# Kernel tuning notes

Measured on AMD Instinct MI355X. Metric: run time of the kernel, lower is better.

The kernel has to match this reference:

```python
import jax, jax.numpy as jnp
import numpy as np

EPS = 1e-6

def _feature_map(x):
    # elu(x) + 1, from https://arxiv.org/pdf/2006.16236.pdf
    return jax.nn.elu(x) + 1.0

def setup_inputs() -> dict:
    key = jax.random.key(0)
    kq, kk, kv = jax.random.split(key, 3)
    N, S, H, D = 4, 4096, 8, 64
    queries = jax.random.normal(kq, (N, S, H, D), dtype=jnp.float32)
    keys = jax.random.normal(kk, (N, S, H, D), dtype=jnp.float32)
    values = jax.random.normal(kv, (N, S, H, D), dtype=jnp.float32)
    q_mask = jnp.ones((N, S), dtype=bool)
    kv_mask = jnp.ones((N, S), dtype=bool)
    return {"queries": queries, "keys": keys, "values": values,
            "q_mask": q_mask, "kv_mask": kv_mask}

def reference(queries, keys, values, q_mask, kv_mask):
    dt = queries.dtype
    q = _feature_map(queries) * q_mask[:, :, None, None].astype(dt)
    k = _feature_map(keys) * kv_mask[:, :, None, None].astype(dt)
    v = values * kv_mask[:, :, None, None].astype(dt)
    L = v.shape[1]
    v = v / L  # normalize for numerical stability, rescaled at the end
    # kv: [N,H,D,V] outer-product aggregation over S2
    kv = jnp.einsum('nshd,nshv->nhdv', k, v)
    # z: [N,L,H] normalizer
    z = 1.0 / (jnp.einsum('nlhd,nhd->nlh', q, k.sum(axis=1)) + EPS)
    out = jnp.einsum('nlhd,nhdv->nlhv', q, kv) * z[..., None] * L
    return out
```

## Files before the change

### kernel.cpp

```cpp
#include <hip/hip_runtime.h>

#define NB    4
#define SEQ   4096
#define NH    8
#define DIM   64
#define NPAIR (NB * NH)
#define SC    256
#define NT    (SC / 64)
#define NCHUNK (SEQ / SC)
#define NLT   (SEQ / 64)
#define VSTR  (NH * DIM)

#define EPSF  1e-6f

__device__ __forceinline__ float fm(float x) {
    return x > 0.0f ? x + 1.0f : __expf(x);
}

#define FMA4(AI, KS) \
    acc[AI][0] = fmaf((KS), v4.x, acc[AI][0]); \
    acc[AI][1] = fmaf((KS), v4.y, acc[AI][1]); \
    acc[AI][2] = fmaf((KS), v4.z, acc[AI][2]); \
    acc[AI][3] = fmaf((KS), v4.w, acc[AI][3]);

template<int ATOMIC>
__global__ __launch_bounds__(256, 2) void la_phase1(
    const float* __restrict__ Kp, const float* __restrict__ Vp,
    float* __restrict__ part,
    float* __restrict__ kspart,
    float* __restrict__ kvfin,
    float* __restrict__ ksfin)
{
    const int chunk = blockIdx.x;
    const int pair  = blockIdx.y;
    const int n = pair >> 3, h = pair & 7;
    const int t     = threadIdx.x;
    const int w     = t >> 6;
    const int lane  = t & 63;
    const int dhalf = w & 1, shalf = w >> 1;
    const int dgrp  = lane >> 4;
    const int vq    = (lane & 15) * 4;
    const int db    = dhalf * 32 + dgrp * 8;
    const int s0    = chunk * SC;

    __shared__ float kbuf[2][64][64];
    __shared__ float vbuf[2][64][64];
    __shared__ float kscr[16][64];

    const int srow = t >> 4, scol = (t & 15) * 4;
    const float* kbase = Kp + ((size_t)((n * SEQ + s0) * NH + h)) * DIM + scol;
    const float* vbase = Vp + ((size_t)((n * SEQ + s0) * NH + h)) * DIM + scol;

    float  ksacc[4] = {0.f, 0.f, 0.f, 0.f};
    float4 kreg[4], vreg[4];

    #pragma unroll
    for (int i = 0; i < 4; ++i) {
        kreg[i] = *(const float4*)(kbase + (size_t)(srow + i * 16) * VSTR);
        vreg[i] = *(const float4*)(vbase + (size_t)(srow + i * 16) * VSTR);
    }
    #pragma unroll
    for (int i = 0; i < 4; ++i) {
        float4 kk = kreg[i];
        kk.x = fm(kk.x); kk.y = fm(kk.y); kk.z = fm(kk.z); kk.w = fm(kk.w);
        ksacc[0] += kk.x; ksacc[1] += kk.y; ksacc[2] += kk.z; ksacc[3] += kk.w;
        *(float4*)&kbuf[0][srow + i * 16][scol] = kk;
        *(float4*)&vbuf[0][srow + i * 16][scol] = vreg[i];
    }
    __syncthreads();

    float acc[8][4] = {};

    for (int tt = 0; tt < NT; ++tt) {
        const int cur = tt & 1;
        if (tt + 1 < NT) {
            const size_t off = (size_t)(tt + 1) * 64;
            #pragma unroll
            for (int i = 0; i < 4; ++i) {
                kreg[i] = *(const float4*)(kbase + (off + srow + i * 16) * VSTR);
                vreg[i] = *(const float4*)(vbase + (off + srow + i * 16) * VSTR);
            }
        }
        __builtin_amdgcn_sched_barrier(0);

        #pragma unroll 8
        for (int ss = 0; ss < 32; ++ss) {
            const int r = shalf * 32 + ss;
            const float4 v4 = *(const float4*)&vbuf[cur][r][vq];
            const float4 k0 = *(const float4*)&kbuf[cur][r][db];
            const float4 k1 = *(const float4*)&kbuf[cur][r][db + 4];
            FMA4(0, k0.x) FMA4(1, k0.y) FMA4(2, k0.z) FMA4(3, k0.w)
            FMA4(4, k1.x) FMA4(5, k1.y) FMA4(6, k1.z) FMA4(7, k1.w)
        }
        __builtin_amdgcn_sched_barrier(0);

        if (tt + 1 < NT) {
            const int nxt = cur ^ 1;
            #pragma unroll
            for (int i = 0; i < 4; ++i) {
                float4 kk = kreg[i];
                kk.x = fm(kk.x); kk.y = fm(kk.y); kk.z = fm(kk.z); kk.w = fm(kk.w);
                ksacc[0] += kk.x; ksacc[1] += kk.y; ksacc[2] += kk.z; ksacc[3] += kk.w;
                *(float4*)&kbuf[nxt][srow + i * 16][scol] = kk;
                *(float4*)&vbuf[nxt][srow + i * 16][scol] = vreg[i];
            }
        }
        __syncthreads();
    }

    *(float4*)&kscr[srow][scol] = make_float4(ksacc[0], ksacc[1], ksacc[2], ksacc[3]);
    __syncthreads();

    if (ATOMIC) {
        float* kvp = kvfin + (size_t)pair * (DIM * DIM);
        #pragma unroll
        for (int i = 0; i < 8; ++i) {
            #pragma unroll
            for (int j = 0; j < 4; ++j)
                atomicAdd(&kvp[(db + i) * DIM + vq + j], acc[i][j]);
        }
        if (t < DIM) {
            float s = 0.0f;
            #pragma unroll
            for (int g = 0; g < 16; ++g) s += kscr[g][t];
            atomicAdd(&ksfin[pair * DIM + t], s);
        }
    } else {
        float* slot = part + ((size_t)pair * (2 * NCHUNK) + chunk * 2 + shalf) * (DIM * DIM);
        #pragma unroll
        for (int i = 0; i < 8; ++i)
            *(float4*)&slot[(db + i) * DIM + vq] =
                make_float4(acc[i][0], acc[i][1], acc[i][2], acc[i][3]);
        if (t < DIM) {
            float s = 0.0f;
            #pragma unroll
            for (int g = 0; g < 16; ++g) s += kscr[g][t];
            kspart[((size_t)pair * NCHUNK + chunk) * DIM + t] = s;
        }
    }
}

__global__ __launch_bounds__(256) void la_reduce(
    const float* __restrict__ part, const float* __restrict__ kspart,
    float* __restrict__ kvfin, float* __restrict__ ksfin)
{
    const int pair = blockIdx.y;
    const int idx  = blockIdx.x * 256 + threadIdx.x;
    const float* p = part + (size_t)pair * (2 * NCHUNK) * (DIM * DIM) + idx;
    float s = 0.0f;
    #pragma unroll 8
    for (int c = 0; c < 2 * NCHUNK; ++c) s += p[(size_t)c * (DIM * DIM)];
    kvfin[(size_t)pair * (DIM * DIM) + idx] = s;

    if (blockIdx.x == 0 && threadIdx.x < DIM) {
        const float* kp = kspart + (size_t)pair * NCHUNK * DIM + threadIdx.x;
        float ks = 0.0f;
        #pragma unroll
        for (int c = 0; c < NCHUNK; ++c) ks += kp[(size_t)c * DIM];
        ksfin[pair * DIM + threadIdx.x] = ks;
    }
}

__global__ __launch_bounds__(256, 4) void la_phase2(
    const float* __restrict__ Qp, const float* __restrict__ kvfin,
    const float* __restrict__ ksfin, float* __restrict__ Outp)
{
    const int ltile = blockIdx.x;
    const int pair  = blockIdx.y;
    const int n = pair >> 3, h = pair & 7;
    const int t    = threadIdx.x;
    const int w    = t >> 6;
    const int lane = t & 63;
    const int lgrp = lane >> 5;
    const int vp   = (lane & 31) * 2;
    const int lb   = w * 16 + lgrp * 8;
    const int l0   = ltile * 64;

    __shared__ float kvs[DIM][DIM];
    __shared__ float qT [DIM][68];
    __shared__ float ksums[DIM];
    __shared__ float zbuf[DIM];

    float qv[16];
    #pragma unroll
    for (int it = 0; it < 4; ++it) {
        const int lr = it * 16 + w * 4;
        #pragma unroll
        for (int i = 0; i < 4; ++i)
            qv[it * 4 + i] =
                Qp[((size_t)((n * SEQ + l0 + lr + i) * NH + h)) * DIM + lane];
    }
    const float* kvp = kvfin + (size_t)pair * (DIM * DIM);
    float4 kvv[4];
    #pragma unroll
    for (int it = 0; it < 4; ++it) {
        const int idx = t + it * 256;
        kvv[it] = *(const float4*)(kvp + (idx >> 4) * DIM + (idx & 15) * 4);
    }
    float ksv = 0.0f;
    if (t < DIM) ksv = ksfin[pair * DIM + t];

    #pragma unroll
    for (int it = 0; it < 4; ++it) {
        const int idx = t + it * 256;
        *(float4*)&kvs[idx >> 4][(idx & 15) * 4] = kvv[it];
    }
    #pragma unroll
    for (int it = 0; it < 4; ++it) {
        const int lr = it * 16 + w * 4;
        *(float4*)&qT[lane][lr] = make_float4(fm(qv[it * 4]),     fm(qv[it * 4 + 1]),
                                              fm(qv[it * 4 + 2]), fm(qv[it * 4 + 3]));
    }
    if (t < DIM) ksums[t] = ksv;
    __syncthreads();

    if (t < DIM) {
        float dot = 0.0f;
        #pragma unroll 8
        for (int k = 0; k < DIM; ++k) dot = fmaf(qT[k][t], ksums[k], dot);
        zbuf[t] = 1.0f / (dot + EPSF);
    }
    __syncthreads();

    float acc[8][2] = {};
    #pragma unroll 4
    for (int k = 0; k < DIM; ++k) {
        const float2 bv = *(const float2*)&kvs[k][vp];
        const float4 a0 = *(const float4*)&qT[k][lb];
        const float4 a1 = *(const float4*)&qT[k][lb + 4];
        acc[0][0] = fmaf(a0.x, bv.x, acc[0][0]); acc[0][1] = fmaf(a0.x, bv.y, acc[0][1]);
        acc[1][0] = fmaf(a0.y, bv.x, acc[1][0]); acc[1][1] = fmaf(a0.y, bv.y, acc[1][1]);
        acc[2][0] = fmaf(a0.z, bv.x, acc[2][0]); acc[2][1] = fmaf(a0.z, bv.y, acc[2][1]);
        acc[3][0] = fmaf(a0.w, bv.x, acc[3][0]); acc[3][1] = fmaf(a0.w, bv.y, acc[3][1]);
        acc[4][0] = fmaf(a1.x, bv.x, acc[4][0]); acc[4][1] = fmaf(a1.x, bv.y, acc[4][1]);
        acc[5][0] = fmaf(a1.y, bv.x, acc[5][0]); acc[5][1] = fmaf(a1.y, bv.y, acc[5][1]);
        acc[6][0] = fmaf(a1.z, bv.x, acc[6][0]); acc[6][1] = fmaf(a1.z, bv.y, acc[6][1]);
        acc[7][0] = fmaf(a1.w, bv.x, acc[7][0]); acc[7][1] = fmaf(a1.w, bv.y, acc[7][1]);
    }

    #pragma unroll
    for (int i = 0; i < 8; ++i) {
        const float z = zbuf[lb + i];
        const int l = l0 + lb + i;
        *(float2*)(Outp + ((size_t)((n * SEQ + l) * NH + h)) * DIM + vp) =
            make_float2(acc[i][0] * z, acc[i][1] * z);
    }
}

extern "C" void kernel_launch(void* const* d_in, const int* in_sizes, int n_in,
                              void* d_out, int out_size, void* d_ws, size_t ws_size,
                              hipStream_t stream) {
    const float* Q = (const float*)d_in[0];
    const float* K = (const float*)d_in[1];
    const float* V = (const float*)d_in[2];
    float* out = (float*)d_out;

    const size_t part_elems  = (size_t)NPAIR * (2 * NCHUNK) * DIM * DIM;
    const size_t kspart_elems = (size_t)NPAIR * NCHUNK * DIM;
    const size_t kv_elems    = (size_t)NPAIR * DIM * DIM;
    const size_t ks_elems    = (size_t)NPAIR * DIM;
    const size_t need = (part_elems + kspart_elems + kv_elems + ks_elems) * sizeof(float);

    if (ws_size >= need) {
        float* part   = (float*)d_ws;
        float* kspart = part + part_elems;
        float* kvfin  = kspart + kspart_elems;
        float* ksfin  = kvfin + kv_elems;
        la_phase1<0><<<dim3(NCHUNK, NPAIR), 256, 0, stream>>>(K, V, part, kspart, kvfin, ksfin);
        la_reduce<<<dim3(16, NPAIR), 256, 0, stream>>>(part, kspart, kvfin, ksfin);
        la_phase2<<<dim3(NLT, NPAIR), 256, 0, stream>>>(Q, kvfin, ksfin, out);
    } else {
        float* kvfin = (float*)d_ws;
        float* ksfin = kvfin + kv_elems;
        hipMemsetAsync(d_ws, 0, (kv_elems + ks_elems) * sizeof(float), stream);
        la_phase1<1><<<dim3(NCHUNK, NPAIR), 256, 0, stream>>>(K, V, nullptr, nullptr, kvfin, ksfin);
        la_phase2<<<dim3(NLT, NPAIR), 256, 0, stream>>>(Q, kvfin, ksfin, out);
    }
}
```

Baseline: 154.8 us.

## Use 8x8 register tiles in both phases with swizzled LDS staging

Phase 1 now gives each thread an 8x8 KV outer-product tile, and each wave handles a quarter of the sequence rows. Partial sums are staged through swizzled shared memory and written as four per-wave slots per chunk, so the reduce kernel sums twice as many partials. Phase 2 processes 256 rows per block, one 64-row tile per wave, with 8x8 register tiles. It folds the normalizer dot product into the main loop and writes output through swizzled LDS for coalesced stores. The aim is more FMAs per LDS load; the costs are higher register pressure, fewer blocks, and extra partial traffic in the reduce.

```diff
diff --git a/kernel.cpp b/kernel.cpp
--- a/kernel.cpp
+++ b/kernel.cpp
@@ -8,7 +8,7 @@
 #define SC    256
 #define NT    (SC / 64)
 #define NCHUNK (SEQ / SC)
-#define NLT   (SEQ / 64)
+#define NLT2  (SEQ / 256)
 #define VSTR  (NH * DIM)
 
 #define EPSF  1e-6f
@@ -17,11 +17,9 @@
     return x > 0.0f ? x + 1.0f : __expf(x);
 }
 
-#define FMA4(AI, KS) \
-    acc[AI][0] = fmaf((KS), v4.x, acc[AI][0]); \
-    acc[AI][1] = fmaf((KS), v4.y, acc[AI][1]); \
-    acc[AI][2] = fmaf((KS), v4.z, acc[AI][2]); \
-    acc[AI][3] = fmaf((KS), v4.w, acc[AI][3]);
+__device__ __forceinline__ int swz(int row) {
+    return ((row & 7) << 3) ^ (((row >> 3) & 3) << 2);
+}
 
 template<int ATOMIC>
 __global__ __launch_bounds__(256, 2) void la_phase1(
@@ -34,18 +32,20 @@
     const int chunk = blockIdx.x;
     const int pair  = blockIdx.y;
     const int n = pair >> 3, h = pair & 7;
-    const int t     = threadIdx.x;
-    const int w     = t >> 6;
-    const int lane  = t & 63;
-    const int dhalf = w & 1, shalf = w >> 1;
-    const int dgrp  = lane >> 4;
-    const int vq    = (lane & 15) * 4;
-    const int db    = dhalf * 32 + dgrp * 8;
-    const int s0    = chunk * SC;
-
-    __shared__ float kbuf[2][64][64];
-    __shared__ float vbuf[2][64][64];
-    __shared__ float kscr[16][64];
+    const int t    = threadIdx.x;
+    const int w    = t >> 6;
+    const int lane = t & 63;
+    const int dgrp = lane >> 3;
+    const int vgrp = lane & 7;
+    const int db   = dgrp * 8;
+    const int vb   = vgrp * 8;
+    const int s0   = chunk * SC;
+
+    __shared__ float smem[2*4096 + 2*4096 + 1024];
+#define KB(b,r,c)  smem[(b)*4096 + (r)*64 + (c)]
+#define VB(b,r,c)  smem[8192 + (b)*4096 + (r)*64 + (c)]
+#define RED(ww,i)  smem[(ww)*4096 + (i)]
+#define KSCR(g,c)  smem[16384 + (g)*64 + (c)]
 
     const int srow = t >> 4, scol = (t & 15) * 4;
     const float* kbase = Kp + ((size_t)((n * SEQ + s0) * NH + h)) * DIM + scol;
@@ -61,36 +61,42 @@
     }
     #pragma unroll
     for (int i = 0; i < 4; ++i) {
-        float4 kk = kreg[i];
-        kk.x = fm(kk.x); kk.y = fm(kk.y); kk.z = fm(kk.z); kk.w = fm(kk.w);
-        ksacc[0] += kk.x; ksacc[1] += kk.y; ksacc[2] += kk.z; ksacc[3] += kk.w;
-        *(float4*)&kbuf[0][srow + i * 16][scol] = kk;
-        *(float4*)&vbuf[0][srow + i * 16][scol] = vreg[i];
+        float4 kk4 = kreg[i];
+        kk4.x = fm(kk4.x); kk4.y = fm(kk4.y); kk4.z = fm(kk4.z); kk4.w = fm(kk4.w);
+        ksacc[0] += kk4.x; ksacc[1] += kk4.y; ksacc[2] += kk4.z; ksacc[3] += kk4.w;
+        *(float4*)&KB(0, srow + i * 16, scol) = kk4;
+        *(float4*)&VB(0, srow + i * 16, scol) = vreg[i];
     }
     __syncthreads();
 
-    float acc[8][4] = {};
+    float acc[8][8] = {};
 
     for (int tt = 0; tt < NT; ++tt) {
         const int cur = tt & 1;
         if (tt + 1 < NT) {
-            const size_t off = (size_t)(tt + 1) * 64;
+            const int off = (tt + 1) * 64;
             #pragma unroll
             for (int i = 0; i < 4; ++i) {
-                kreg[i] = *(const float4*)(kbase + (off + srow + i * 16) * VSTR);
-                vreg[i] = *(const float4*)(vbase + (off + srow + i * 16) * VSTR);
+                kreg[i] = *(const float4*)(kbase + (size_t)(off + srow + i * 16) * VSTR);
+                vreg[i] = *(const float4*)(vbase + (size_t)(off + srow + i * 16) * VSTR);
             }
         }
         __builtin_amdgcn_sched_barrier(0);
 
-        #pragma unroll 8
-        for (int ss = 0; ss < 32; ++ss) {
-            const int r = shalf * 32 + ss;
-            const float4 v4 = *(const float4*)&vbuf[cur][r][vq];
-            const float4 k0 = *(const float4*)&kbuf[cur][r][db];
-            const float4 k1 = *(const float4*)&kbuf[cur][r][db + 4];
-            FMA4(0, k0.x) FMA4(1, k0.y) FMA4(2, k0.z) FMA4(3, k0.w)
-            FMA4(4, k1.x) FMA4(5, k1.y) FMA4(6, k1.z) FMA4(7, k1.w)
+        #pragma unroll
+        for (int ss = 0; ss < 16; ++ss) {
+            const int r = w * 16 + ss;
+            const float4 k0 = *(const float4*)&KB(cur, r, db);
+            const float4 k1 = *(const float4*)&KB(cur, r, db + 4);
+            const float4 v0 = *(const float4*)&VB(cur, r, vb);
+            const float4 v1 = *(const float4*)&VB(cur, r, vb + 4);
+            const float kk[8] = {k0.x,k0.y,k0.z,k0.w,k1.x,k1.y,k1.z,k1.w};
+            const float vv[8] = {v0.x,v0.y,v0.z,v0.w,v1.x,v1.y,v1.z,v1.w};
+            #pragma unroll
+            for (int i = 0; i < 8; ++i)
+                #pragma unroll
+                for (int j = 0; j < 8; ++j)
+                    acc[i][j] = fmaf(kk[i], vv[j], acc[i][j]);
         }
         __builtin_amdgcn_sched_barrier(0);
 
@@ -98,46 +104,63 @@
             const int nxt = cur ^ 1;
             #pragma unroll
             for (int i = 0; i < 4; ++i) {
-                float4 kk = kreg[i];
-                kk.x = fm(kk.x); kk.y = fm(kk.y); kk.z = fm(kk.z); kk.w = fm(kk.w);
-                ksacc[0] += kk.x; ksacc[1] += kk.y; ksacc[2] += kk.z; ksacc[3] += kk.w;
-                *(float4*)&kbuf[nxt][srow + i * 16][scol] = kk;
-                *(float4*)&vbuf[nxt][srow + i * 16][scol] = vreg[i];
+                float4 kk4 = kreg[i];
+                kk4.x = fm(kk4.x); kk4.y = fm(kk4.y); kk4.z = fm(kk4.z); kk4.w = fm(kk4.w);
+                ksacc[0] += kk4.x; ksacc[1] += kk4.y; ksacc[2] += kk4.z; ksacc[3] += kk4.w;
+                *(float4*)&KB(nxt, srow + i * 16, scol) = kk4;
+                *(float4*)&VB(nxt, srow + i * 16, scol) = vreg[i];
             }
         }
         __syncthreads();
     }
 
-    *(float4*)&kscr[srow][scol] = make_float4(ksacc[0], ksacc[1], ksacc[2], ksacc[3]);
-    __syncthreads();
+    *(float4*)&KSCR(srow, scol) = make_float4(ksacc[0], ksacc[1], ksacc[2], ksacc[3]);
 
     if (ATOMIC) {
+        __syncthreads();
         float* kvp = kvfin + (size_t)pair * (DIM * DIM);
         #pragma unroll
-        for (int i = 0; i < 8; ++i) {
-            #pragma unroll
-            for (int j = 0; j < 4; ++j)
-                atomicAdd(&kvp[(db + i) * DIM + vq + j], acc[i][j]);
-        }
+        for (int i = 0; i < 8; ++i)
+            #pragma unroll
+            for (int j = 0; j < 8; ++j)
+                atomicAdd(&kvp[(db + i) * DIM + vb + j], acc[i][j]);
         if (t < DIM) {
             float s = 0.0f;
             #pragma unroll
-            for (int g = 0; g < 16; ++g) s += kscr[g][t];
+            for (int g = 0; g < 16; ++g) s += KSCR(g, t);
             atomicAdd(&ksfin[pair * DIM + t], s);
         }
     } else {
-        float* slot = part + ((size_t)pair * (2 * NCHUNK) + chunk * 2 + shalf) * (DIM * DIM);
-        #pragma unroll
-        for (int i = 0; i < 8; ++i)
-            *(float4*)&slot[(db + i) * DIM + vq] =
-                make_float4(acc[i][0], acc[i][1], acc[i][2], acc[i][3]);
+        #pragma unroll
+        for (int i = 0; i < 8; ++i) {
+            const int row = db + i;
+            const int sw = swz(row);
+            #pragma unroll
+            for (int jj = 0; jj < 2; ++jj)
+                *(float4*)&RED(w, row * 64 + ((vb + jj * 4) ^ sw)) =
+                    make_float4(acc[i][jj*4], acc[i][jj*4+1], acc[i][jj*4+2], acc[i][jj*4+3]);
+        }
+        __syncthreads();
+        float* slot = part + (((size_t)pair * NCHUNK + chunk) * 4 + w) * (DIM * DIM);
+        #pragma unroll
+        for (int jj = 0; jj < 16; ++jj) {
+            const int g = jj * 64 + lane;
+            const int row = g >> 4;
+            const int col = (g & 15) * 4;
+            const float4 v4 = *(const float4*)&RED(w, row * 64 + (col ^ swz(row)));
+            *(float4*)(slot + g * 4) = v4;
+        }
         if (t < DIM) {
             float s = 0.0f;
             #pragma unroll
-            for (int g = 0; g < 16; ++g) s += kscr[g][t];
+            for (int g = 0; g < 16; ++g) s += KSCR(g, t);
             kspart[((size_t)pair * NCHUNK + chunk) * DIM + t] = s;
         }
     }
+#undef KB
+#undef VB
+#undef RED
+#undef KSCR
 }
 
 __global__ __launch_bounds__(256) void la_reduce(
@@ -146,10 +169,10 @@
 {
     const int pair = blockIdx.y;
     const int idx  = blockIdx.x * 256 + threadIdx.x;
-    const float* p = part + (size_t)pair * (2 * NCHUNK) * (DIM * DIM) + idx;
+    const float* p = part + (size_t)pair * (NCHUNK * 4) * (DIM * DIM) + idx;
     float s = 0.0f;
     #pragma unroll 8
-    for (int c = 0; c < 2 * NCHUNK; ++c) s += p[(size_t)c * (DIM * DIM)];
+    for (int c = 0; c < NCHUNK * 4; ++c) s += p[(size_t)c * (DIM * DIM)];
     kvfin[(size_t)pair * (DIM * DIM) + idx] = s;
 
     if (blockIdx.x == 0 && threadIdx.x < DIM) {
@@ -161,90 +184,94 @@
     }
 }
 
-__global__ __launch_bounds__(256, 4) void la_phase2(
+__global__ __launch_bounds__(256, 2) void la_phase2(
     const float* __restrict__ Qp, const float* __restrict__ kvfin,
     const float* __restrict__ ksfin, float* __restrict__ Outp)
 {
-    const int ltile = blockIdx.x;
-    const int pair  = blockIdx.y;
+    const int lchunk = blockIdx.x;
+    const int pair   = blockIdx.y;
     const int n = pair >> 3, h = pair & 7;
     const int t    = threadIdx.x;
     const int w    = t >> 6;
     const int lane = t & 63;
-    const int lgrp = lane >> 5;
-    const int vp   = (lane & 31) * 2;
-    const int lb   = w * 16 + lgrp * 8;
-    const int l0   = ltile * 64;
-
-    __shared__ float kvs[DIM][DIM];
-    __shared__ float qT [DIM][68];
-    __shared__ float ksums[DIM];
-    __shared__ float zbuf[DIM];
-
-    float qv[16];
+    const int lgrp = lane >> 3;
+    const int vgrp = lane & 7;
+    const int lb   = lgrp * 8;
+    const int vb   = vgrp * 8;
+    const int l0   = lchunk * 256 + w * 64;
+
+    __shared__ float smem2[4096 + 4 * 4096];
+#define KVS(i)    smem2[(i)]
+#define QT(ww,i)  smem2[4096 + (ww)*4096 + (i)]
+
+    const float* kvp = kvfin + (size_t)pair * (DIM * DIM);
     #pragma unroll
     for (int it = 0; it < 4; ++it) {
-        const int lr = it * 16 + w * 4;
-        #pragma unroll
-        for (int i = 0; i < 4; ++i)
-            qv[it * 4 + i] =
-                Qp[((size_t)((n * SEQ + l0 + lr + i) * NH + h)) * DIM + lane];
-    }
-    const float* kvp = kvfin + (size_t)pair * (DIM * DIM);
-    float4 kvv[4];
-    #pragma unroll
-    for (int it = 0; it < 4; ++it) {
-        const int idx = t + it * 256;
-        kvv[it] = *(const float4*)(kvp + (idx >> 4) * DIM + (idx & 15) * 4);
-    }
-    float ksv = 0.0f;
-    if (t < DIM) ksv = ksfin[pair * DIM + t];
-
-    #pragma unroll
-    for (int it = 0; it < 4; ++it) {
-        const int idx = t + it * 256;
-        *(float4*)&kvs[idx >> 4][(idx & 15) * 4] = kvv[it];
-    }
-    #pragma unroll
-    for (int it = 0; it < 4; ++it) {
-        const int lr = it * 16 + w * 4;
-        *(float4*)&qT[lane][lr] = make_float4(fm(qv[it * 4]),     fm(qv[it * 4 + 1]),
-                                              fm(qv[it * 4 + 2]), fm(qv[it * 4 + 3]));
-    }
-    if (t < DIM) ksums[t] = ksv;
+        const int g = t + it * 256;
+        *(float4*)&KVS(g * 4) = *(const float4*)(kvp + g * 4);
+    }
+
+    {
+        const int sw = swz(lane);
+        for (int c = 0; c < 4; ++c) {
+            float qv[16];
+            #pragma unroll
+            for (int i = 0; i < 16; ++i)
+                qv[i] = Qp[((size_t)((n * SEQ + l0 + c * 16 + i) * NH + h)) * DIM + lane];
+            #pragma unroll
+            for (int mi = 0; mi < 4; ++mi) {
+                const int lbase = c * 16 + mi * 4;
+                *(float4*)&QT(w, lane * 64 + (lbase ^ sw)) =
+                    make_float4(fm(qv[mi*4]), fm(qv[mi*4+1]), fm(qv[mi*4+2]), fm(qv[mi*4+3]));
+            }
+        }
+    }
     __syncthreads();
 
-    if (t < DIM) {
-        float dot = 0.0f;
-        #pragma unroll 8
-        for (int k = 0; k < DIM; ++k) dot = fmaf(qT[k][t], ksums[k], dot);
-        zbuf[t] = 1.0f / (dot + EPSF);
-    }
-    __syncthreads();
-
-    float acc[8][2] = {};
-    #pragma unroll 4
+    float acc[8][8] = {};
+    float zac[8] = {};
+    const float* ksp = ksfin + pair * DIM;
+
+    #pragma unroll 8
     for (int k = 0; k < DIM; ++k) {
-        const float2 bv = *(const float2*)&kvs[k][vp];
-        const float4 a0 = *(const float4*)&qT[k][lb];
-        const float4 a1 = *(const float4*)&qT[k][lb + 4];
-        acc[0][0] = fmaf(a0.x, bv.x, acc[0][0]); acc[0][1] = fmaf(a0.x, bv.y, acc[0][1]);
-        acc[1][0] = fmaf(a0.y, bv.x, acc[1][0]); acc[1][1] = fmaf(a0.y, bv.y, acc[1][1]);
-        acc[2][0] = fmaf(a0.z, bv.x, acc[2][0]); acc[2][1] = fmaf(a0.z, bv.y, acc[2][1]);
-        acc[3][0] = fmaf(a0.w, bv.x, acc[3][0]); acc[3][1] = fmaf(a0.w, bv.y, acc[3][1]);
-        acc[4][0] = fmaf(a1.x, bv.x, acc[4][0]); acc[4][1] = fmaf(a1.x, bv.y, acc[4][1]);
-        acc[5][0] = fmaf(a1.y, bv.x, acc[5][0]); acc[5][1] = fmaf(a1.y, bv.y, acc[5][1]);
-        acc[6][0] = fmaf(a1.z, bv.x, acc[6][0]); acc[6][1] = fmaf(a1.z, bv.y, acc[6][1]);
-        acc[7][0] = fmaf(a1.w, bv.x, acc[7][0]); acc[7][1] = fmaf(a1.w, bv.y, acc[7][1]);
+        const int sk = swz(k);
+        const float4 a0 = *(const float4*)&QT(w, k * 64 + (lb ^ sk));
+        const float4 a1 = *(const float4*)&QT(w, k * 64 + ((lb + 4) ^ sk));
+        const float4 b0 = *(const float4*)&KVS(k * 64 + vb);
+        const float4 b1 = *(const float4*)&KVS(k * 64 + vb + 4);
+        const float ksk = ksp[k];
+        const float qq[8]  = {a0.x,a0.y,a0.z,a0.w,a1.x,a1.y,a1.z,a1.w};
+        const float vvv[8] = {b0.x,b0.y,b0.z,b0.w,b1.x,b1.y,b1.z,b1.w};
+        #pragma unroll
+        for (int i = 0; i < 8; ++i) {
+            zac[i] = fmaf(qq[i], ksk, zac[i]);
+            #pragma unroll
+            for (int j = 0; j < 8; ++j)
+                acc[i][j] = fmaf(qq[i], vvv[j], acc[i][j]);
+        }
     }
 
     #pragma unroll
     for (int i = 0; i < 8; ++i) {
-        const float z = zbuf[lb + i];
-        const int l = l0 + lb + i;
-        *(float2*)(Outp + ((size_t)((n * SEQ + l) * NH + h)) * DIM + vp) =
-            make_float2(acc[i][0] * z, acc[i][1] * z);
-    }
+        const float z = 1.0f / (zac[i] + EPSF);
+        const int row = lb + i;
+        const int sw = swz(row);
+        #pragma unroll
+        for (int jj = 0; jj < 2; ++jj)
+            *(float4*)&QT(w, row * 64 + ((vb + jj * 4) ^ sw)) =
+                make_float4(acc[i][jj*4] * z, acc[i][jj*4+1] * z,
+                            acc[i][jj*4+2] * z, acc[i][jj*4+3] * z);
+    }
+    #pragma unroll
+    for (int jj = 0; jj < 16; ++jj) {
+        const int g = jj * 64 + lane;
+        const int row = g >> 4;
+        const int col = (g & 15) * 4;
+        const float4 v4 = *(const float4*)&QT(w, row * 64 + (col ^ swz(row)));
+        *(float4*)(Outp + ((size_t)((n * SEQ + l0 + row) * NH + h)) * DIM + col) = v4;
+    }
+#undef KVS
+#undef QT
 }
 
 extern "C" void kernel_launch(void* const* d_in, const int* in_sizes, int n_in,
@@ -255,10 +282,10 @@
     const float* V = (const float*)d_in[2];
     float* out = (float*)d_out;
 
-    const size_t part_elems  = (size_t)NPAIR * (2 * NCHUNK) * DIM * DIM;
+    const size_t part_elems   = (size_t)NPAIR * NCHUNK * 4 * DIM * DIM;
     const size_t kspart_elems = (size_t)NPAIR * NCHUNK * DIM;
-    const size_t kv_elems    = (size_t)NPAIR * DIM * DIM;
-    const size_t ks_elems    = (size_t)NPAIR * DIM;
+    const size_t kv_elems     = (size_t)NPAIR * DIM * DIM;
+    const size_t ks_elems     = (size_t)NPAIR * DIM;
     const size_t need = (part_elems + kspart_elems + kv_elems + ks_elems) * sizeof(float);
 
     if (ws_size >= need) {
@@ -268,12 +295,12 @@
         float* ksfin  = kvfin + kv_elems;
         la_phase1<0><<<dim3(NCHUNK, NPAIR), 256, 0, stream>>>(K, V, part, kspart, kvfin, ksfin);
         la_reduce<<<dim3(16, NPAIR), 256, 0, stream>>>(part, kspart, kvfin, ksfin);
-        la_phase2<<<dim3(NLT, NPAIR), 256, 0, stream>>>(Q, kvfin, ksfin, out);
+        la_phase2<<<dim3(NLT2, NPAIR), 256, 0, stream>>>(Q, kvfin, ksfin, out);
     } else {
         float* kvfin = (float*)d_ws;
         float* ksfin = kvfin + kv_elems;
         hipMemsetAsync(d_ws, 0, (kv_elems + ks_elems) * sizeof(float), stream);
         la_phase1<1><<<dim3(NCHUNK, NPAIR), 256, 0, stream>>>(K, V, nullptr, nullptr, kvfin, ksfin);
-        la_phase2<<<dim3(NLT, NPAIR), 256, 0, stream>>>(Q, kvfin, ksfin, out);
-    }
-}
+        la_phase2<<<dim3(NLT2, NPAIR), 256, 0, stream>>>(Q, kvfin, ksfin, out);
+    }
+}
```

After: 282.1 us. +82.2%, slower.
